# Optimization experiments

Hardware: AMD Instinct MI355X
Metric: run time of the kernel (lower is better)

The kernel has to match this reference:

```python
import jax, jax.numpy as jnp
import numpy as np

N, C, H, W, SF = 4, 3, 1024, 1024, 4


def setup_inputs() -> dict:
    key = jax.random.key(0)
    ks = jax.random.split(key, 6)
    z = jax.random.normal(ks[0], (N, C, H, W), dtype=jnp.float32)
    Fk = jax.random.normal(ks[1], (N, C, H, W, 2), dtype=jnp.float32)
    FkC = jax.random.normal(ks[2], (N, C, H, W, 2), dtype=jnp.float32)
    F2k = jax.random.normal(ks[3], (N, C, H, W, 2), dtype=jnp.float32)
    FkCFy = jax.random.normal(ks[4], (N, C, H, W, 2), dtype=jnp.float32)
    # alpha is a positive penalty weight; keep it away from 0 (it divides FX)
    alpha = jax.random.uniform(ks[5], (N, 1, 1, 1), dtype=jnp.float32,
                               minval=0.1, maxval=1.0)
    return {"z": z, "Fk": Fk, "FkC": FkC, "F2k": F2k,
            "FkCFy": FkCFy, "alpha": alpha, "sf": SF}


def _toc(t):
    # [..., 2] real/imag pair (old torch.rfft onesided=False layout) -> complex
    return jax.lax.complex(t[..., 0], t[..., 1])


def _block_mean(a, sf):
    # torch splits() + mean over the sf*sf blocks == mean over an sf-strided
    # block decomposition of the H and W axes (order of blocks is irrelevant
    # under the mean). a: (N, C, H, W) complex -> (N, C, H//sf, W//sf)
    n, c, h, w = a.shape
    return a.reshape(n, c, sf, h // sf, sf, w // sf).mean(axis=(2, 4))


def reference(z, Fk, FkC, F2k, FkCFy, alpha, sf):
    # torch.rfft(x, 2, onesided=False) == full 2-D FFT over last two dims
    FR = _toc(FkCFy) + jnp.fft.fft2(alpha * z)                  # (N,C,H,W) complex
    FBR = _block_mean(_toc(Fk) * FR, sf)                        # (N,C,H/sf,W/sf)
    invW = _block_mean(_toc(F2k), sf)                           # (N,C,H/sf,W/sf)
    invWBR = FBR / (invW + alpha)                               # csum adds alpha to real part
    FCBinvWBR = _toc(FkC) * jnp.tile(invWBR, (1, 1, sf, sf))    # torch .repeat == tile
    FX = (FR - FCBinvWBR) / alpha
    # torch.irfft(FX, 2, onesided=False) == real part of inverse 2-D FFT
    return jnp.real(jnp.fft.ifft2(FX))
```

## Files before the change

### kernel.cpp

```cpp
#include <hip/hip_runtime.h>
#include <cmath>

#define HN 1024
#define NCH 12
#define PI2 6.28318530717958647692f

__device__ __forceinline__ float2 cmul(float2 a, float2 b) {
  return make_float2(a.x * b.x - a.y * b.y, a.x * b.y + a.y * b.x);
}

__device__ __forceinline__ int drev(int k) {
  int r = 0;
#pragma unroll
  for (int i = 0; i < 5; ++i) { r = (r << 2) | (k & 3); k >>= 2; }
  return r;
}

__device__ __forceinline__ int aswz(int h, int w) { return w ^ ((h & 63) << 4); }

#define RIDX(h) ((h) + ((h) >> 4))
#define TIDX(i) ((i) + ((i) >> 4))
#define EIDX(h, c) ((h) * 17 + (c))

template <bool INV>
__device__ __forceinline__ void bf4(float2& a0, float2& a1, float2& a2, float2& a3,
                                    const float2* tw, int e) {
  float2 t0 = make_float2(a0.x + a2.x, a0.y + a2.y);
  float2 t1 = make_float2(a0.x - a2.x, a0.y - a2.y);
  float2 t2 = make_float2(a1.x + a3.x, a1.y + a3.y);
  float2 t3 = make_float2(a1.x - a3.x, a1.y - a3.y);
  float2 b0 = make_float2(t0.x + t2.x, t0.y + t2.y);
  float2 b2 = make_float2(t0.x - t2.x, t0.y - t2.y);
  float2 b1, b3;
  if (!INV) {
    b1 = make_float2(t1.x + t3.y, t1.y - t3.x);
    b3 = make_float2(t1.x - t3.y, t1.y + t3.x);
  } else {
    b1 = make_float2(t1.x - t3.y, t1.y + t3.x);
    b3 = make_float2(t1.x + t3.y, t1.y - t3.x);
  }
  float2 w1 = tw[e], w2 = tw[2 * e], w3 = tw[3 * e];
  if (INV) { w1.y = -w1.y; w2.y = -w2.y; w3.y = -w3.y; }
  a0 = b0;
  a1 = cmul(b1, w1);
  a2 = cmul(b2, w2);
  a3 = cmul(b3, w3);
}

template <bool INV>
__device__ __forceinline__ void bf4t(float2& a0, float2& a1, float2& a2, float2& a3,
                                     const float2* tw, int e) {
  float2 t0 = make_float2(a0.x + a2.x, a0.y + a2.y);
  float2 t1 = make_float2(a0.x - a2.x, a0.y - a2.y);
  float2 t2 = make_float2(a1.x + a3.x, a1.y + a3.y);
  float2 t3 = make_float2(a1.x - a3.x, a1.y - a3.y);
  float2 b0 = make_float2(t0.x + t2.x, t0.y + t2.y);
  float2 b2 = make_float2(t0.x - t2.x, t0.y - t2.y);
  float2 b1, b3;
  if (!INV) {
    b1 = make_float2(t1.x + t3.y, t1.y - t3.x);
    b3 = make_float2(t1.x - t3.y, t1.y + t3.x);
  } else {
    b1 = make_float2(t1.x - t3.y, t1.y + t3.x);
    b3 = make_float2(t1.x + t3.y, t1.y - t3.x);
  }
  float2 w1 = tw[TIDX(e)], w2 = tw[TIDX(2 * e)], w3 = tw[TIDX(3 * e)];
  if (INV) { w1.y = -w1.y; w2.y = -w2.y; w3.y = -w3.y; }
  a0 = b0;
  a1 = cmul(b1, w1);
  a2 = cmul(b2, w2);
  a3 = cmul(b3, w3);
}

__device__ __forceinline__ void tw_init(float2* tw, int t, int nthr) {
  for (int i = t; i < 768; i += nthr) {
    float s, c;
    sincosf((float)i * (PI2 / 1024.f), &s, &c);
    tw[i] = make_float2(c, -s);
  }
}

__device__ __forceinline__ void tw_init_p(float2* tw, int t, int nthr) {
  for (int i = t; i < 768; i += nthr) {
    float s, c;
    sincosf((float)i * (PI2 / 1024.f), &s, &c);
    tw[TIDX(i)] = make_float2(c, -s);
  }
}

template <bool INV>
__device__ __forceinline__ void fft_row(float2* x, const float2* tw, int t) {
#pragma unroll
  for (int ld = 8; ld >= 0; ld -= 2) {
    __syncthreads();
    const int d = 1 << ld;
    int j = t & (d - 1);
    int p0 = ((t >> ld) << (ld + 2)) | j;
    float2 a0 = x[RIDX(p0)];
    float2 a1 = x[RIDX(p0 + d)];
    float2 a2 = x[RIDX(p0 + 2 * d)];
    float2 a3 = x[RIDX(p0 + 3 * d)];
    bf4<INV>(a0, a1, a2, a3, tw, j << (8 - ld));
    x[RIDX(p0)] = a0;
    x[RIDX(p0 + d)] = a1;
    x[RIDX(p0 + 2 * d)] = a2;
    x[RIDX(p0 + 3 * d)] = a3;
  }
  __syncthreads();
}

template <bool INV>
__device__ __forceinline__ void colfft16(float2 (&r)[16], float2 (&q)[16],
                                         float2* ex, const float2* tw,
                                         int u, int c) {
  const int j2 = u & 3, B = u >> 2;
#pragma unroll
  for (int s = 0; s < 4; ++s)
    bf4t<INV>(r[s], r[s + 4], r[s + 8], r[s + 12], tw, u + (s << 6));
#pragma unroll
  for (int g = 0; g < 4; ++g)
    bf4t<INV>(r[4 * g], r[4 * g + 1], r[4 * g + 2], r[4 * g + 3], tw, u << 2);
#pragma unroll
  for (int it = 0; it < 8; ++it)
    ex[EIDX(u + (it << 6), c)] = r[it];
  __syncthreads();
  if (u < 32) {
#pragma unroll
    for (int m = 0; m < 16; ++m) {
      int hl = (B << 6) + j2 + ((m & 3) << 2) + ((m >> 2) << 4);
      q[m] = ex[EIDX(hl, c)];
    }
  }
  __syncthreads();
#pragma unroll
  for (int it = 8; it < 16; ++it)
    ex[EIDX(u + (it << 6) - 512, c)] = r[it];
  __syncthreads();
  if (u >= 32) {
#pragma unroll
    for (int m = 0; m < 16; ++m) {
      int hl = ((B - 8) << 6) + j2 + ((m & 3) << 2) + ((m >> 2) << 4);
      q[m] = ex[EIDX(hl, c)];
    }
  }
#pragma unroll
  for (int a = 0; a < 4; ++a)
    bf4t<INV>(q[a], q[4 + a], q[8 + a], q[12 + a], tw, (j2 + 4 * a) << 4);
#pragma unroll
  for (int b_ = 0; b_ < 4; ++b_)
    bf4t<INV>(q[4 * b_], q[4 * b_ + 1], q[4 * b_ + 2], q[4 * b_ + 3], tw, j2 << 6);
#pragma unroll
  for (int m = 0; m < 16; ++m) {
    float2 v = q[m];
    float2 p;
    p.x = __shfl_xor(v.x, 32);
    p.y = __shfl_xor(v.y, 32);
    float2 w;
    if (j2 & 2) { w.x = p.x - v.x; w.y = p.y - v.y; }
    else        { w.x = v.x + p.x; w.y = v.y + p.y; }
    float2 p2;
    p2.x = __shfl_xor(w.x, 16);
    p2.y = __shfl_xor(w.y, 16);
    float2 o;
    if (j2 == 0)      { o = make_float2(w.x + p2.x, w.y + p2.y); }
    else if (j2 == 1) { o = make_float2(p2.x - w.x, p2.y - w.y); }
    else if (j2 == 2) { o = INV ? make_float2(w.x - p2.y, w.y + p2.x)
                                : make_float2(w.x + p2.y, w.y - p2.x); }
    else              { o = INV ? make_float2(p2.x + w.y, p2.y - w.x)
                                : make_float2(p2.x - w.y, p2.y + w.x); }
    q[m] = o;
  }
}

__global__ __launch_bounds__(256) void k1_rowfft(const float* __restrict__ z,
                                                 const float* __restrict__ alpha,
                                                 float2* __restrict__ A) {
  __shared__ float2 x[1088];
  __shared__ float2 tw[768];
  const int t = threadIdx.x;
  const int row = blockIdx.x, nc = blockIdx.y;
  tw_init(tw, t, 256);
  const float al = alpha[nc / 3];
  const float4* zr4 = (const float4*)(z + ((size_t)nc * HN + row) * HN);
  {
    float4 v = zr4[t];
    int h = t << 2;
    x[RIDX(h + 0)] = make_float2(v.x * al, 0.f);
    x[RIDX(h + 1)] = make_float2(v.y * al, 0.f);
    x[RIDX(h + 2)] = make_float2(v.z * al, 0.f);
    x[RIDX(h + 3)] = make_float2(v.w * al, 0.f);
  }
  fft_row<false>(x, tw, t);
  float4* Ar4 = (float4*)(A + (size_t)nc * HN * HN + (size_t)row * HN);
  const int X = (row & 63) << 4;
#pragma unroll
  for (int half = 0; half < 2; ++half) {
    int k0 = (half << 9) | (t << 1);
    float2 a = x[RIDX(drev(k0))];
    float2 b = x[RIDX(drev(k0 | 1))];
    Ar4[(k0 ^ X) >> 1] = make_float4(a.x, a.y, b.x, b.y);
  }
}

__global__ __launch_bounds__(1024, 4) void k2_colfft(float2* __restrict__ A,
                                                     const float2* __restrict__ FkCFy,
                                                     const float2* __restrict__ Fk,
                                                     float2* __restrict__ P) {
  __shared__ float2 ex[8704];
  __shared__ float2 tw[816];
  const int t = threadIdx.x;
  const int c = t & 15, u = t >> 4;
  const int w0 = blockIdx.x << 4;
  const int nc = blockIdx.y;
  const size_t base = (size_t)nc * HN * HN;
  float2 r[16], q[16];
#pragma unroll
  for (int it = 0; it < 16; ++it) {
    int h = u + (it << 6);
    r[it] = A[base + (size_t)h * HN + (aswz(h, w0) + c)];
  }
  tw_init_p(tw, t, 1024);
  __syncthreads();
  colfft16<false>(r, q, ex, tw, u, c);
  const int j2 = u & 3, B = u >> 2;
  const int f = ((j2 & 1) << 1) | (j2 >> 1);
  float2* Pp = P + (((size_t)nc) << 18) + w0 + c;
#pragma unroll
  for (int m = 0; m < 16; ++m) {
    int klo = ((m & 3) << 6) | ((m >> 2) << 4) | ((B & 3) << 2) | (B >> 2);
    int k = (f << 8) | klo;
    float2 fy = FkCFy[base + (size_t)k * HN + w0 + c];
    float2 fr = make_float2(q[m].x + fy.x, q[m].y + fy.y);
    A[base + (size_t)k * HN + (aswz(k, w0) + c)] = fr;
    float2 fk = Fk[base + (size_t)k * HN + w0 + c];
    float2 pr = cmul(fk, fr);
    pr.x += __shfl_xor(pr.x, 16);
    pr.y += __shfl_xor(pr.y, 16);
    pr.x += __shfl_xor(pr.x, 32);
    pr.y += __shfl_xor(pr.y, 32);
    if (j2 == 0) Pp[(size_t)klo << 10] = pr;
  }
}

__global__ __launch_bounds__(256) void k3_reduce(const float2* __restrict__ P,
                                                 const float2* __restrict__ F2k,
                                                 const float* __restrict__ alpha,
                                                 float2* __restrict__ iw) {
  int idx = blockIdx.x * 256 + threadIdx.x;
  int j = idx & 255, i = (idx >> 8) & 255, nc = idx >> 16;
  size_t base = (size_t)nc * HN * HN;
  float wx = 0.f, wy = 0.f;
#pragma unroll
  for (int s1 = 0; s1 < 4; ++s1) {
#pragma unroll
    for (int s2 = 0; s2 < 4; ++s2) {
      float2 f2 = F2k[base + (size_t)((s1 << 8) + i) * HN + ((s2 << 8) + j)];
      wx += f2.x;
      wy += f2.y;
    }
  }
  const float2* Pp = P + (((size_t)nc) << 18) + ((size_t)i << 10);
  float sx = 0.f, sy = 0.f;
#pragma unroll
  for (int s2 = 0; s2 < 4; ++s2) {
    float2 p = Pp[(s2 << 8) + j];
    sx += p.x;
    sy += p.y;
  }
  const float al = alpha[nc / 3];
  float dx = wx * 0.0625f + al, dy = wy * 0.0625f;
  float nx = sx * 0.0625f, ny = sy * 0.0625f;
  float inv = 1.0f / (dx * dx + dy * dy);
  iw[idx] = make_float2((nx * dx + ny * dy) * inv, (ny * dx - nx * dy) * inv);
}

__global__ __launch_bounds__(1024, 4) void k4_colifft(float2* __restrict__ A,
                                                      const float2* __restrict__ FkC,
                                                      const float2* __restrict__ iw,
                                                      const float* __restrict__ alpha) {
  __shared__ float2 ex[8704];
  __shared__ float2 tw[816];
  const int t = threadIdx.x;
  const int c = t & 15, u = t >> 4;
  const int w0 = blockIdx.x << 4;
  const int nc = blockIdx.y;
  const float al = alpha[nc / 3];
  const float ra = 1.0f / al;
  const size_t base = (size_t)nc * HN * HN;
  const int jcol = (w0 + c) & 255;
  const float2* iwp = iw + ((size_t)nc << 16);
  float2 r[16], q[16];
#pragma unroll
  for (int it = 0; it < 16; ++it) {
    int h = u + (it << 6);
    float2 fr = A[base + (size_t)h * HN + (aswz(h, w0) + c)];
    float2 fc = FkC[base + (size_t)h * HN + w0 + c];
    float2 w = iwp[((h & 255) << 8) | jcol];
    float2 p = cmul(fc, w);
    r[it] = make_float2((fr.x - p.x) * ra, (fr.y - p.y) * ra);
  }
  tw_init_p(tw, t, 1024);
  __syncthreads();
  colfft16<true>(r, q, ex, tw, u, c);
  const int j2 = u & 3, B = u >> 2;
  const int f = ((j2 & 1) << 1) | (j2 >> 1);
#pragma unroll
  for (int m = 0; m < 16; ++m) {
    int k = (f << 8) | ((m & 3) << 6) | ((m >> 2) << 4) | ((B & 3) << 2) | (B >> 2);
    A[base + (size_t)k * HN + (aswz(k, w0) + c)] = q[m];
  }
}

__global__ __launch_bounds__(256) void k5_rowifft(const float2* __restrict__ A,
                                                  float* __restrict__ out) {
  __shared__ float2 x[1088];
  __shared__ float2 tw[768];
  const int t = threadIdx.x;
  const int row = blockIdx.x, nc = blockIdx.y;
  tw_init(tw, t, 256);
  const float4* Ar4 = (const float4*)(A + (size_t)nc * HN * HN + (size_t)row * HN);
  const int X = (row & 63) << 4;
#pragma unroll
  for (int half = 0; half < 2; ++half) {
    int h0 = (half << 9) | (t << 1);
    float4 v = Ar4[(h0 ^ X) >> 1];
    x[RIDX(h0)] = make_float2(v.x, v.y);
    x[RIDX(h0 | 1)] = make_float2(v.z, v.w);
  }
  fft_row<true>(x, tw, t);
  float4* outr4 = (float4*)(out + ((size_t)nc * HN + row) * HN);
  const float sc = 1.0f / (1024.0f * 1024.0f);
  {
    int k = t << 2;
    float4 o;
    o.x = x[RIDX(drev(k + 0))].x * sc;
    o.y = x[RIDX(drev(k + 1))].x * sc;
    o.z = x[RIDX(drev(k + 2))].x * sc;
    o.w = x[RIDX(drev(k + 3))].x * sc;
    outr4[t] = o;
  }
}

extern "C" void kernel_launch(void* const* d_in, const int* in_sizes, int n_in,
                              void* d_out, int out_size, void* d_ws, size_t ws_size,
                              hipStream_t stream) {
  const float*  z      = (const float*)d_in[0];
  const float2* Fk     = (const float2*)d_in[1];
  const float2* FkC    = (const float2*)d_in[2];
  const float2* F2k    = (const float2*)d_in[3];
  const float2* FkCFy  = (const float2*)d_in[4];
  const float*  alpha  = (const float*)d_in[5];
  (void)in_sizes; (void)n_in; (void)out_size; (void)ws_size;

  float2* A  = (float2*)d_ws;
  float2* iw = A + (size_t)NCH * HN * HN;
  float2* P  = iw + (size_t)NCH * 256 * 256;
  float*  out = (float*)d_out;

  k1_rowfft<<<dim3(HN, NCH), dim3(256), 0, stream>>>(z, alpha, A);
  k2_colfft<<<dim3(HN / 16, NCH), dim3(1024), 0, stream>>>(A, FkCFy, Fk, P);
  k3_reduce<<<dim3(NCH * 256), dim3(256), 0, stream>>>(P, F2k, alpha, iw);
  k4_colifft<<<dim3(HN / 16, NCH), dim3(1024), 0, stream>>>(A, FkC, iw, alpha);
  k5_rowifft<<<dim3(HN, NCH), dim3(256), 0, stream>>>(A, out);
}
```

Before: 291.9 us.

## Move Fk*FR block reduction out of column FFT into separate reduce kernel

```diff
diff --git a/kernel.cpp b/kernel.cpp
--- a/kernel.cpp
+++ b/kernel.cpp
@@ -172,6 +172,24 @@
   }
 }
 
+__global__ __launch_bounds__(256) void k3a_w(const float2* __restrict__ F2k,
+                                             float2* __restrict__ w2) {
+  int idx = blockIdx.x * 256 + threadIdx.x;
+  int j = idx & 255, i = (idx >> 8) & 255, nc = idx >> 16;
+  size_t base = (size_t)nc * HN * HN;
+  float wx = 0.f, wy = 0.f;
+#pragma unroll
+  for (int s1 = 0; s1 < 4; ++s1) {
+#pragma unroll
+    for (int s2 = 0; s2 < 4; ++s2) {
+      float2 f2 = F2k[base + (size_t)((s1 << 8) + i) * HN + ((s2 << 8) + j)];
+      wx += f2.x;
+      wy += f2.y;
+    }
+  }
+  w2[idx] = make_float2(wx, wy);
+}
+
 __global__ __launch_bounds__(256) void k1_rowfft(const float* __restrict__ z,
                                                  const float* __restrict__ alpha,
                                                  float2* __restrict__ A) {
@@ -203,9 +221,7 @@
 }
 
 __global__ __launch_bounds__(1024, 4) void k2_colfft(float2* __restrict__ A,
-                                                     const float2* __restrict__ FkCFy,
-                                                     const float2* __restrict__ Fk,
-                                                     float2* __restrict__ P) {
+                                                     const float2* __restrict__ FkCFy) {
   __shared__ float2 ex[8704];
   __shared__ float2 tw[816];
   const int t = threadIdx.x;
@@ -224,51 +240,38 @@
   colfft16<false>(r, q, ex, tw, u, c);
   const int j2 = u & 3, B = u >> 2;
   const int f = ((j2 & 1) << 1) | (j2 >> 1);
-  float2* Pp = P + (((size_t)nc) << 18) + w0 + c;
 #pragma unroll
   for (int m = 0; m < 16; ++m) {
-    int klo = ((m & 3) << 6) | ((m >> 2) << 4) | ((B & 3) << 2) | (B >> 2);
-    int k = (f << 8) | klo;
+    int k = (f << 8) | ((m & 3) << 6) | ((m >> 2) << 4) | ((B & 3) << 2) | (B >> 2);
     float2 fy = FkCFy[base + (size_t)k * HN + w0 + c];
-    float2 fr = make_float2(q[m].x + fy.x, q[m].y + fy.y);
-    A[base + (size_t)k * HN + (aswz(k, w0) + c)] = fr;
-    float2 fk = Fk[base + (size_t)k * HN + w0 + c];
-    float2 pr = cmul(fk, fr);
-    pr.x += __shfl_xor(pr.x, 16);
-    pr.y += __shfl_xor(pr.y, 16);
-    pr.x += __shfl_xor(pr.x, 32);
-    pr.y += __shfl_xor(pr.y, 32);
-    if (j2 == 0) Pp[(size_t)klo << 10] = pr;
-  }
-}
-
-__global__ __launch_bounds__(256) void k3_reduce(const float2* __restrict__ P,
-                                                 const float2* __restrict__ F2k,
-                                                 const float* __restrict__ alpha,
-                                                 float2* __restrict__ iw) {
+    A[base + (size_t)k * HN + (aswz(k, w0) + c)] =
+        make_float2(q[m].x + fy.x, q[m].y + fy.y);
+  }
+}
+
+__global__ __launch_bounds__(256) void k3b_iw(const float2* __restrict__ A,
+                                              const float2* __restrict__ Fk,
+                                              const float2* __restrict__ w2,
+                                              const float* __restrict__ alpha,
+                                              float2* __restrict__ iw) {
   int idx = blockIdx.x * 256 + threadIdx.x;
   int j = idx & 255, i = (idx >> 8) & 255, nc = idx >> 16;
   size_t base = (size_t)nc * HN * HN;
-  float wx = 0.f, wy = 0.f;
+  float sx = 0.f, sy = 0.f;
 #pragma unroll
   for (int s1 = 0; s1 < 4; ++s1) {
 #pragma unroll
     for (int s2 = 0; s2 < 4; ++s2) {
-      float2 f2 = F2k[base + (size_t)((s1 << 8) + i) * HN + ((s2 << 8) + j)];
-      wx += f2.x;
-      wy += f2.y;
+      int h = (s1 << 8) + i, w = (s2 << 8) + j;
+      float2 fr = A[base + (size_t)h * HN + aswz(h, w)];
+      float2 fk = Fk[base + (size_t)h * HN + w];
+      sx += fk.x * fr.x - fk.y * fr.y;
+      sy += fk.x * fr.y + fk.y * fr.x;
     }
   }
-  const float2* Pp = P + (((size_t)nc) << 18) + ((size_t)i << 10);
-  float sx = 0.f, sy = 0.f;
-#pragma unroll
-  for (int s2 = 0; s2 < 4; ++s2) {
-    float2 p = Pp[(s2 << 8) + j];
-    sx += p.x;
-    sy += p.y;
-  }
   const float al = alpha[nc / 3];
-  float dx = wx * 0.0625f + al, dy = wy * 0.0625f;
+  float2 wv = w2[idx];
+  float dx = wv.x * 0.0625f + al, dy = wv.y * 0.0625f;
   float nx = sx * 0.0625f, ny = sy * 0.0625f;
   float inv = 1.0f / (dx * dx + dy * dy);
   iw[idx] = make_float2((nx * dx + ny * dy) * inv, (ny * dx - nx * dy) * inv);
@@ -354,12 +357,13 @@
 
   float2* A  = (float2*)d_ws;
   float2* iw = A + (size_t)NCH * HN * HN;
-  float2* P  = iw + (size_t)NCH * 256 * 256;
+  float2* w2 = iw + (size_t)NCH * 256 * 256;
   float*  out = (float*)d_out;
 
+  k3a_w<<<dim3(NCH * 256), dim3(256), 0, stream>>>(F2k, w2);
   k1_rowfft<<<dim3(HN, NCH), dim3(256), 0, stream>>>(z, alpha, A);
-  k2_colfft<<<dim3(HN / 16, NCH), dim3(1024), 0, stream>>>(A, FkCFy, Fk, P);
-  k3_reduce<<<dim3(NCH * 256), dim3(256), 0, stream>>>(P, F2k, alpha, iw);
+  k2_colfft<<<dim3(HN / 16, NCH), dim3(1024), 0, stream>>>(A, FkCFy);
+  k3b_iw<<<dim3(NCH * 256), dim3(256), 0, stream>>>(A, Fk, w2, alpha, iw);
   k4_colifft<<<dim3(HN / 16, NCH), dim3(1024), 0, stream>>>(A, FkC, iw, alpha);
   k5_rowifft<<<dim3(HN, NCH), dim3(256), 0, stream>>>(A, out);
 }
```

New measurement: 277.4 us. 5.0% less time.

## Exploit Hermitian symmetry of real-input FFTs to halve column-FFT work

Applied to the files above, without the earlier changes.

```diff
diff --git a/kernel.cpp b/kernel.cpp
--- a/kernel.cpp
+++ b/kernel.cpp
@@ -3,6 +3,7 @@
 
 #define HN 1024
 #define NCH 12
+#define AS 528
 #define PI2 6.28318530717958647692f
 
 __device__ __forceinline__ float2 cmul(float2 a, float2 b) {
@@ -15,8 +16,6 @@
   for (int i = 0; i < 5; ++i) { r = (r << 2) | (k & 3); k >>= 2; }
   return r;
 }
-
-__device__ __forceinline__ int aswz(int h, int w) { return w ^ ((h & 63) << 4); }
 
 #define RIDX(h) ((h) + ((h) >> 4))
 #define TIDX(i) ((i) + ((i) >> 4))
@@ -174,7 +173,7 @@
 
 __global__ __launch_bounds__(256) void k1_rowfft(const float* __restrict__ z,
                                                  const float* __restrict__ alpha,
-                                                 float2* __restrict__ A) {
+                                                 float2* __restrict__ Ah) {
   __shared__ float2 x[1088];
   __shared__ float2 tw[768];
   const int t = threadIdx.x;
@@ -191,81 +190,76 @@
     x[RIDX(h + 3)] = make_float2(v.w * al, 0.f);
   }
   fft_row<false>(x, tw, t);
-  float4* Ar4 = (float4*)(A + (size_t)nc * HN * HN + (size_t)row * HN);
-  const int X = (row & 63) << 4;
-#pragma unroll
-  for (int half = 0; half < 2; ++half) {
-    int k0 = (half << 9) | (t << 1);
+  float2* Ar = Ah + ((size_t)nc * HN + row) * AS;
+  float4* Ar4 = (float4*)Ar;
+  {
+    int k0 = t << 1;
     float2 a = x[RIDX(drev(k0))];
     float2 b = x[RIDX(drev(k0 | 1))];
-    Ar4[(k0 ^ X) >> 1] = make_float4(a.x, a.y, b.x, b.y);
-  }
-}
-
-__global__ __launch_bounds__(1024, 4) void k2_colfft(float2* __restrict__ A,
-                                                     const float2* __restrict__ FkCFy,
-                                                     const float2* __restrict__ Fk,
-                                                     float2* __restrict__ P) {
+    Ar4[t] = make_float4(a.x, a.y, b.x, b.y);
+  }
+  if (t == 0) Ar[512] = x[RIDX(drev(512))];
+}
+
+__global__ __launch_bounds__(1024, 4) void k2_colfft(float2* __restrict__ Ah) {
   __shared__ float2 ex[8704];
   __shared__ float2 tw[816];
   const int t = threadIdx.x;
   const int c = t & 15, u = t >> 4;
   const int w0 = blockIdx.x << 4;
   const int nc = blockIdx.y;
-  const size_t base = (size_t)nc * HN * HN;
+  const size_t rb = (size_t)nc * HN;
   float2 r[16], q[16];
 #pragma unroll
   for (int it = 0; it < 16; ++it) {
     int h = u + (it << 6);
-    r[it] = A[base + (size_t)h * HN + (aswz(h, w0) + c)];
+    r[it] = Ah[(rb + h) * AS + w0 + c];
   }
   tw_init_p(tw, t, 1024);
   __syncthreads();
   colfft16<false>(r, q, ex, tw, u, c);
   const int j2 = u & 3, B = u >> 2;
   const int f = ((j2 & 1) << 1) | (j2 >> 1);
-  float2* Pp = P + (((size_t)nc) << 18) + w0 + c;
 #pragma unroll
   for (int m = 0; m < 16; ++m) {
-    int klo = ((m & 3) << 6) | ((m >> 2) << 4) | ((B & 3) << 2) | (B >> 2);
-    int k = (f << 8) | klo;
-    float2 fy = FkCFy[base + (size_t)k * HN + w0 + c];
-    float2 fr = make_float2(q[m].x + fy.x, q[m].y + fy.y);
-    A[base + (size_t)k * HN + (aswz(k, w0) + c)] = fr;
-    float2 fk = Fk[base + (size_t)k * HN + w0 + c];
-    float2 pr = cmul(fk, fr);
-    pr.x += __shfl_xor(pr.x, 16);
-    pr.y += __shfl_xor(pr.y, 16);
-    pr.x += __shfl_xor(pr.x, 32);
-    pr.y += __shfl_xor(pr.y, 32);
-    if (j2 == 0) Pp[(size_t)klo << 10] = pr;
-  }
-}
-
-__global__ __launch_bounds__(256) void k3_reduce(const float2* __restrict__ P,
+    int k = (f << 8) | ((m & 3) << 6) | ((m >> 2) << 4) | ((B & 3) << 2) | (B >> 2);
+    Ah[(rb + k) * AS + w0 + c] = q[m];
+  }
+}
+
+__global__ __launch_bounds__(256) void k3_reduce(const float2* __restrict__ Ah,
+                                                 const float2* __restrict__ Fk,
+                                                 const float2* __restrict__ FkCFy,
                                                  const float2* __restrict__ F2k,
                                                  const float* __restrict__ alpha,
                                                  float2* __restrict__ iw) {
   int idx = blockIdx.x * 256 + threadIdx.x;
   int j = idx & 255, i = (idx >> 8) & 255, nc = idx >> 16;
   size_t base = (size_t)nc * HN * HN;
-  float wx = 0.f, wy = 0.f;
+  size_t rb = (size_t)nc * HN;
+  float sx = 0.f, sy = 0.f, wx = 0.f, wy = 0.f;
 #pragma unroll
   for (int s1 = 0; s1 < 4; ++s1) {
+    int h = (s1 << 8) + i;
+    int h2 = (1024 - h) & 1023;
 #pragma unroll
     for (int s2 = 0; s2 < 4; ++s2) {
-      float2 f2 = F2k[base + (size_t)((s1 << 8) + i) * HN + ((s2 << 8) + j)];
+      int w = (s2 << 8) + j;
+      size_t gi = base + (size_t)h * HN + w;
+      float2 fk = Fk[gi];
+      float2 fy = FkCFy[gi];
+      float2 f2 = F2k[gi];
+      bool mir = (w > 512);
+      int col = mir ? 1024 - w : w;
+      int row = mir ? h2 : h;
+      float2 g = Ah[(rb + row) * AS + col];
+      if (mir) g.y = -g.y;
+      float2 fr = make_float2(fy.x + g.x, fy.y + g.y);
+      sx += fk.x * fr.x - fk.y * fr.y;
+      sy += fk.x * fr.y + fk.y * fr.x;
       wx += f2.x;
       wy += f2.y;
     }
-  }
-  const float2* Pp = P + (((size_t)nc) << 18) + ((size_t)i << 10);
-  float sx = 0.f, sy = 0.f;
-#pragma unroll
-  for (int s2 = 0; s2 < 4; ++s2) {
-    float2 p = Pp[(s2 << 8) + j];
-    sx += p.x;
-    sy += p.y;
   }
   const float al = alpha[nc / 3];
   float dx = wx * 0.0625f + al, dy = wy * 0.0625f;
@@ -274,7 +268,8 @@
   iw[idx] = make_float2((nx * dx + ny * dy) * inv, (ny * dx - nx * dy) * inv);
 }
 
-__global__ __launch_bounds__(1024, 4) void k4_colifft(float2* __restrict__ A,
+__global__ __launch_bounds__(1024, 4) void k4_colifft(float2* __restrict__ Ah,
+                                                      const float2* __restrict__ FkCFy,
                                                       const float2* __restrict__ FkC,
                                                       const float2* __restrict__ iw,
                                                       const float* __restrict__ alpha) {
@@ -284,20 +279,30 @@
   const int c = t & 15, u = t >> 4;
   const int w0 = blockIdx.x << 4;
   const int nc = blockIdx.y;
-  const float al = alpha[nc / 3];
-  const float ra = 1.0f / al;
+  const float ra = 0.5f / alpha[nc / 3];
   const size_t base = (size_t)nc * HN * HN;
-  const int jcol = (w0 + c) & 255;
+  const size_t rb = (size_t)nc * HN;
+  const int k = w0 + c;
+  const int kc = (1024 - k) & 1023;
   const float2* iwp = iw + ((size_t)nc << 16);
+  const int jd = k & 255, jm = kc & 255;
   float2 r[16], q[16];
 #pragma unroll
   for (int it = 0; it < 16; ++it) {
     int h = u + (it << 6);
-    float2 fr = A[base + (size_t)h * HN + (aswz(h, w0) + c)];
-    float2 fc = FkC[base + (size_t)h * HN + w0 + c];
-    float2 w = iwp[((h & 255) << 8) | jcol];
-    float2 p = cmul(fc, w);
-    r[it] = make_float2((fr.x - p.x) * ra, (fr.y - p.y) * ra);
+    int h2 = (1024 - h) & 1023;
+    size_t gd = base + (size_t)h * HN + k;
+    float2 fy = FkCFy[gd];
+    float2 fc = FkC[gd];
+    float2 wd = iwp[((h & 255) << 8) | jd];
+    float2 pd = cmul(fc, wd);
+    size_t gm = base + (size_t)h2 * HN + kc;
+    float2 fym = FkCFy[gm];
+    float2 fcm = FkC[gm];
+    float2 wm = iwp[((h2 & 255) << 8) | jm];
+    float2 pm = cmul(fcm, wm);
+    r[it] = make_float2((fy.x - pd.x + fym.x - pm.x) * ra,
+                        (fy.y - pd.y - fym.y + pm.y) * ra);
   }
   tw_init_p(tw, t, 1024);
   __syncthreads();
@@ -306,37 +311,51 @@
   const int f = ((j2 & 1) << 1) | (j2 >> 1);
 #pragma unroll
   for (int m = 0; m < 16; ++m) {
-    int k = (f << 8) | ((m & 3) << 6) | ((m >> 2) << 4) | ((B & 3) << 2) | (B >> 2);
-    A[base + (size_t)k * HN + (aswz(k, w0) + c)] = q[m];
-  }
-}
-
-__global__ __launch_bounds__(256) void k5_rowifft(const float2* __restrict__ A,
+    int kr = (f << 8) | ((m & 3) << 6) | ((m >> 2) << 4) | ((B & 3) << 2) | (B >> 2);
+    Ah[(rb + kr) * AS + k] = q[m];
+  }
+}
+
+__global__ __launch_bounds__(256) void k5_rowifft(const float2* __restrict__ Ah,
+                                                  const float* __restrict__ z,
                                                   float* __restrict__ out) {
   __shared__ float2 x[1088];
   __shared__ float2 tw[768];
   const int t = threadIdx.x;
   const int row = blockIdx.x, nc = blockIdx.y;
   tw_init(tw, t, 256);
-  const float4* Ar4 = (const float4*)(A + (size_t)nc * HN * HN + (size_t)row * HN);
-  const int X = (row & 63) << 4;
-#pragma unroll
-  for (int half = 0; half < 2; ++half) {
-    int h0 = (half << 9) | (t << 1);
-    float4 v = Ar4[(h0 ^ X) >> 1];
-    x[RIDX(h0)] = make_float2(v.x, v.y);
-    x[RIDX(h0 | 1)] = make_float2(v.z, v.w);
+  const float2* Ar = Ah + ((size_t)nc * HN + row) * AS;
+  const float4* Ar4 = (const float4*)Ar;
+  {
+    float4 v = Ar4[t];
+    int k0 = t << 1;
+    x[RIDX(k0)] = make_float2(v.x, v.y);
+    x[RIDX(k0 | 1)] = make_float2(v.z, v.w);
+  }
+  if (t == 0) x[RIDX(512)] = Ar[512];
+  __syncthreads();
+  {
+    int k = 513 + t;
+    float2 g = x[RIDX(1024 - k)];
+    x[RIDX(k)] = make_float2(g.x, -g.y);
+  }
+  if (t < 255) {
+    int k = 769 + t;
+    float2 g = x[RIDX(1024 - k)];
+    x[RIDX(k)] = make_float2(g.x, -g.y);
   }
   fft_row<true>(x, tw, t);
+  const float4* zr4 = (const float4*)(z + ((size_t)nc * HN + row) * HN);
   float4* outr4 = (float4*)(out + ((size_t)nc * HN + row) * HN);
   const float sc = 1.0f / (1024.0f * 1024.0f);
   {
+    float4 zv = zr4[t];
     int k = t << 2;
     float4 o;
-    o.x = x[RIDX(drev(k + 0))].x * sc;
-    o.y = x[RIDX(drev(k + 1))].x * sc;
-    o.z = x[RIDX(drev(k + 2))].x * sc;
-    o.w = x[RIDX(drev(k + 3))].x * sc;
+    o.x = x[RIDX(drev(k + 0))].x * sc + zv.x;
+    o.y = x[RIDX(drev(k + 1))].x * sc + zv.y;
+    o.z = x[RIDX(drev(k + 2))].x * sc + zv.z;
+    o.w = x[RIDX(drev(k + 3))].x * sc + zv.w;
     outr4[t] = o;
   }
 }
@@ -352,14 +371,13 @@
   const float*  alpha  = (const float*)d_in[5];
   (void)in_sizes; (void)n_in; (void)out_size; (void)ws_size;
 
-  float2* A  = (float2*)d_ws;
-  float2* iw = A + (size_t)NCH * HN * HN;
-  float2* P  = iw + (size_t)NCH * 256 * 256;
+  float2* Ah = (float2*)d_ws;
+  float2* iw = Ah + (size_t)NCH * HN * AS;
   float*  out = (float*)d_out;
 
-  k1_rowfft<<<dim3(HN, NCH), dim3(256), 0, stream>>>(z, alpha, A);
-  k2_colfft<<<dim3(HN / 16, NCH), dim3(1024), 0, stream>>>(A, FkCFy, Fk, P);
-  k3_reduce<<<dim3(NCH * 256), dim3(256), 0, stream>>>(P, F2k, alpha, iw);
-  k4_colifft<<<dim3(HN / 16, NCH), dim3(1024), 0, stream>>>(A, FkC, iw, alpha);
-  k5_rowifft<<<dim3(HN, NCH), dim3(256), 0, stream>>>(A, out);
-}
+  k1_rowfft<<<dim3(HN, NCH), dim3(256), 0, stream>>>(z, alpha, Ah);
+  k2_colfft<<<dim3(33, NCH), dim3(1024), 0, stream>>>(Ah);
+  k3_reduce<<<dim3(NCH * 256), dim3(256), 0, stream>>>(Ah, Fk, FkCFy, F2k, alpha, iw);
+  k4_colifft<<<dim3(33, NCH), dim3(1024), 0, stream>>>(Ah, FkCFy, FkC, iw, alpha);
+  k5_rowifft<<<dim3(HN, NCH), dim3(256), 0, stream>>>(Ah, z, out);
+}
```

Result: slower. 347.1 us (+18.9%).
